# Kernel optimization log

Hardware: AMD Instinct MI355X
Metric: run time of the kernel (lower is better)

## Reference

```python
import jax, jax.numpy as jnp
import numpy as np


def setup_inputs() -> dict:
    key = jax.random.key(0)
    kq, kk, kv = jax.random.split(key, 3)
    N, L, S, H, D = 4, 2048, 2048, 8, 64
    queries = jax.random.normal(kq, (N, L, H, D), dtype=jnp.float32)
    keys = jax.random.normal(kk, (N, S, H, D), dtype=jnp.float32)
    values = jax.random.normal(kv, (N, S, H, D), dtype=jnp.float32)
    return {"queries": queries, "keys": keys, "values": values}


def reference(queries, keys, values):
    # QK^T: [N, L, S, H]
    qk = jnp.einsum('nlhd,nshd->nlsh', queries, keys)
    softmax_temp = 1.0 / np.sqrt(queries.shape[3]).astype(np.float32)
    attn = jax.nn.softmax(softmax_temp * qk, axis=2)  # softmax over S
    # dropout with drop_rate=0.0 is identity
    out = jnp.einsum('nlsh,nshd->nlhd', attn, values)
    return out
```

## Files before the change

kernel.cpp:

```cpp
#include <hip/hip_runtime.h>
#include <hip/hip_bf16.h>
#include <stdint.h>


typedef __bf16 bf16x8 __attribute__((ext_vector_type(8)));
typedef float  f32x16 __attribute__((ext_vector_type(16)));
typedef float  f32x2  __attribute__((ext_vector_type(2)));

#define QBLK 128
#define NT32 64
#define TILE32 4096
#define PLANE_BF16 (NT32 * TILE32)
#define SCALE_LOG2E 0.18033688011112042f

static __device__ __forceinline__ uint32_t pkbf(float lo, float hi) {
    uint16_t l = __builtin_bit_cast(uint16_t, (__bf16)lo);
    uint16_t h = __builtin_bit_cast(uint16_t, (__bf16)hi);
    return (uint32_t)l | ((uint32_t)h << 16);
}

static __device__ __forceinline__ bf16x8 packP8(float a0, float a1, float a2, float a3,
                                                float a4, float a5, float a6, float a7) {
    uint32_t x0 = pkbf(a0, a1), x1 = pkbf(a2, a3);
    uint32_t y0 = pkbf(a4, a5), y1 = pkbf(a6, a7);
    asm volatile("v_permlane32_swap_b32 %0, %1" : "+v"(x0), "+v"(y0));
    asm volatile("v_permlane32_swap_b32 %0, %1" : "+v"(x1), "+v"(y1));
    union { uint32_t u[4]; bf16x8 v; } pu;
    pu.u[0] = x0; pu.u[1] = x1; pu.u[2] = y0; pu.u[3] = y1;
    return pu.v;
}

__global__ __launch_bounds__(256) void prep(const float* __restrict__ K,
                                            const float* __restrict__ V,
                                            __bf16* __restrict__ F) {
    __shared__ __align__(16) __bf16 T[64 * 64];
    const int tid = threadIdx.x;
    if (blockIdx.x < 2048) {
        const int ch   = blockIdx.x * 256 + tid;
        const int nh   = ch >> 14;
        const int r    = ch & 16383;
        const int t    = r >> 8;
        const int rr   = r & 255;
        const int sl   = rr >> 3;
        const int slot = rr & 7;
        const int n = nh >> 3, h = nh & 7;
        const float* p = K + ((size_t)(n * 2048 + t * 32 + sl) * 8 + h) * 64 + slot * 8;
        float4 a = *(const float4*)p;
        float4 b = *(const float4*)(p + 4);
        bf16x8 v;
        v[0] = (__bf16)a.x; v[1] = (__bf16)a.y; v[2] = (__bf16)a.z; v[3] = (__bf16)a.w;
        v[4] = (__bf16)b.x; v[5] = (__bf16)b.y; v[6] = (__bf16)b.z; v[7] = (__bf16)b.w;
        const int ks = slot >> 1, hh = slot & 1;
        *(bf16x8*)(F + (size_t)nh * PLANE_BF16 + t * TILE32
                     + ks * 512 + (hh * 32 + sl) * 8) = v;
    } else {
        const int bid = blockIdx.x - 2048;
        const int nh  = bid >> 5;
        const int t0  = (bid & 31) * 2;
        const int n   = nh >> 3, h = nh & 7;
        const int s0  = (bid & 31) * 64;
#pragma unroll
        for (int it = 0; it < 16; ++it) {
            const int idx = it * 256 + tid;
            const int sl  = idx >> 6;
            const int d   = idx & 63;
            float v = V[(size_t)(n * 2048 + s0 + sl) * 512 + h * 64 + d];
            T[d * 64 + (((sl >> 3) ^ (d & 7)) * 8) + (sl & 7)] = (__bf16)v;
        }
        __syncthreads();
#pragma unroll
        for (int it = 0; it < 2; ++it) {
            const int idx = it * 256 + tid;
            const int d   = idx >> 3;
            const int sc  = idx & 7;
            bf16x8 v = *(const bf16x8*)&T[d * 64 + ((sc ^ (d & 7)) * 8)];
            const int dt = d >> 5, c = d & 31;
            const int tile = t0 + (sc >> 2), kt = (sc >> 1) & 1, hh = sc & 1;
            *(bf16x8*)(F + (size_t)nh * PLANE_BF16 + tile * TILE32
                         + (4 + dt * 2 + kt) * 512 + (hh * 32 + c) * 8) = v;
        }
    }
}

__global__ __launch_bounds__(512, 4) void fattn(const float* __restrict__ Q,
                                                const __bf16* __restrict__ F,
                                                float* __restrict__ Out) {
    __shared__ __align__(16) float Olds[4][32][64];
    __shared__ float Llds[8][32];

    const int tid  = threadIdx.x;
    const int wv   = tid >> 6;
    const int lane = tid & 63;
    const int hh   = lane >> 5;
    const int c    = lane & 31;
    const int part = wv >> 2;
    const int wq   = wv & 3;

    int bid = blockIdx.x;
    bid = (bid & 7) * 64 + (bid >> 3);
    const int nh = bid >> 4;
    const int qt = bid & 15;
    const int n  = nh >> 3, hd = nh & 7;
    const int q0 = qt * QBLK;
    const int t0 = part * 32;

    const float*  Qp = Q + (size_t)n * 1048576 + hd * 64;
    const bf16x8* Tb = (const bf16x8*)(F + (size_t)nh * PLANE_BF16);

    bf16x8 qf[4];
    {
        const float* qp = Qp + (size_t)(q0 + wq * 32 + c) * 512;
#pragma unroll
        for (int ks = 0; ks < 4; ++ks) {
            float4 a = *(const float4*)(qp + ks * 16 + hh * 8);
            float4 b = *(const float4*)(qp + ks * 16 + hh * 8 + 4);
            bf16x8 v;
            v[0] = (__bf16)(a.x * SCALE_LOG2E); v[1] = (__bf16)(a.y * SCALE_LOG2E);
            v[2] = (__bf16)(a.z * SCALE_LOG2E); v[3] = (__bf16)(a.w * SCALE_LOG2E);
            v[4] = (__bf16)(b.x * SCALE_LOG2E); v[5] = (__bf16)(b.y * SCALE_LOG2E);
            v[6] = (__bf16)(b.z * SCALE_LOG2E); v[7] = (__bf16)(b.w * SCALE_LOG2E);
            qf[ks] = v;
        }
    }

    f32x2 la0 = {0.f, 0.f}, la1 = {0.f, 0.f}, la2 = {0.f, 0.f}, la3 = {0.f, 0.f};
    f32x16 oacc[2];
#pragma unroll
    for (int dt = 0; dt < 2; ++dt)
#pragma unroll
        for (int r = 0; r < 16; ++r) oacc[dt][r] = 0.f;

    bf16x8 kA[4], vv[4];
#pragma unroll
    for (int f = 0; f < 4; ++f) {
        kA[f] = Tb[(size_t)t0 * 512 + f * 64 + lane];
        vv[f] = Tb[(size_t)t0 * 512 + 256 + f * 64 + lane];
    }

#pragma unroll 1
    for (int t = t0; t < t0 + 31; ++t) {
        f32x16 sacc;
#pragma unroll
        for (int r = 0; r < 16; ++r) sacc[r] = 0.f;
        __builtin_amdgcn_s_setprio(1);
#pragma unroll
        for (int ks = 0; ks < 4; ++ks)
            sacc = __builtin_amdgcn_mfma_f32_32x32x16_bf16(kA[ks], qf[ks], sacc, 0, 0, 0);
        __builtin_amdgcn_s_setprio(0);
#pragma unroll
        for (int f = 0; f < 4; ++f) kA[f] = Tb[(size_t)(t + 1) * 512 + f * 64 + lane];

#pragma unroll
        for (int r = 0; r < 8; ++r) sacc[r] = __builtin_amdgcn_exp2f(sacc[r]);
        bf16x8 pf0 = packP8(sacc[0], sacc[1], sacc[2], sacc[3],
                            sacc[4], sacc[5], sacc[6], sacc[7]);
        __builtin_amdgcn_s_setprio(1);
        oacc[0] = __builtin_amdgcn_mfma_f32_32x32x16_bf16(vv[0], pf0, oacc[0], 0, 0, 0);
        oacc[1] = __builtin_amdgcn_mfma_f32_32x32x16_bf16(vv[2], pf0, oacc[1], 0, 0, 0);
        __builtin_amdgcn_s_setprio(0);

#pragma unroll
        for (int r = 8; r < 16; ++r) sacc[r] = __builtin_amdgcn_exp2f(sacc[r]);
        bf16x8 pf1 = packP8(sacc[8],  sacc[9],  sacc[10], sacc[11],
                            sacc[12], sacc[13], sacc[14], sacc[15]);
        __builtin_amdgcn_s_setprio(1);
        oacc[0] = __builtin_amdgcn_mfma_f32_32x32x16_bf16(vv[1], pf1, oacc[0], 0, 0, 0);
        oacc[1] = __builtin_amdgcn_mfma_f32_32x32x16_bf16(vv[3], pf1, oacc[1], 0, 0, 0);
        __builtin_amdgcn_s_setprio(0);

        la0 += f32x2{sacc[0], sacc[1]} + f32x2{sacc[8],  sacc[9]};
        la1 += f32x2{sacc[2], sacc[3]} + f32x2{sacc[10], sacc[11]};
        la2 += f32x2{sacc[4], sacc[5]} + f32x2{sacc[12], sacc[13]};
        la3 += f32x2{sacc[6], sacc[7]} + f32x2{sacc[14], sacc[15]};

#pragma unroll
        for (int f = 0; f < 4; ++f) vv[f] = Tb[(size_t)(t + 1) * 512 + 256 + f * 64 + lane];
    }
    {
        f32x16 sacc;
#pragma unroll
        for (int r = 0; r < 16; ++r) sacc[r] = 0.f;
        __builtin_amdgcn_s_setprio(1);
#pragma unroll
        for (int ks = 0; ks < 4; ++ks)
            sacc = __builtin_amdgcn_mfma_f32_32x32x16_bf16(kA[ks], qf[ks], sacc, 0, 0, 0);
        __builtin_amdgcn_s_setprio(0);
#pragma unroll
        for (int r = 0; r < 8; ++r) sacc[r] = __builtin_amdgcn_exp2f(sacc[r]);
        bf16x8 pf0 = packP8(sacc[0], sacc[1], sacc[2], sacc[3],
                            sacc[4], sacc[5], sacc[6], sacc[7]);
        __builtin_amdgcn_s_setprio(1);
        oacc[0] = __builtin_amdgcn_mfma_f32_32x32x16_bf16(vv[0], pf0, oacc[0], 0, 0, 0);
        oacc[1] = __builtin_amdgcn_mfma_f32_32x32x16_bf16(vv[2], pf0, oacc[1], 0, 0, 0);
        __builtin_amdgcn_s_setprio(0);
#pragma unroll
        for (int r = 8; r < 16; ++r) sacc[r] = __builtin_amdgcn_exp2f(sacc[r]);
        bf16x8 pf1 = packP8(sacc[8],  sacc[9],  sacc[10], sacc[11],
                            sacc[12], sacc[13], sacc[14], sacc[15]);
        __builtin_amdgcn_s_setprio(1);
        oacc[0] = __builtin_amdgcn_mfma_f32_32x32x16_bf16(vv[1], pf1, oacc[0], 0, 0, 0);
        oacc[1] = __builtin_amdgcn_mfma_f32_32x32x16_bf16(vv[3], pf1, oacc[1], 0, 0, 0);
        __builtin_amdgcn_s_setprio(0);
        la0 += f32x2{sacc[0], sacc[1]} + f32x2{sacc[8],  sacc[9]};
        la1 += f32x2{sacc[2], sacc[3]} + f32x2{sacc[10], sacc[11]};
        la2 += f32x2{sacc[4], sacc[5]} + f32x2{sacc[12], sacc[13]};
        la3 += f32x2{sacc[6], sacc[7]} + f32x2{sacc[14], sacc[15]};
    }

    la0 += la1; la2 += la3; la0 += la2;
    float lsum = la0[0] + la0[1];
    lsum += __shfl_xor(lsum, 32, 64);
    if (hh == 0) Llds[wv][c] = lsum;
    if (part == 1) {
#pragma unroll
        for (int dt = 0; dt < 2; ++dt) {
#pragma unroll
            for (int rr = 0; rr < 4; ++rr) {
                const int s = dt * 8 + rr * 2 + hh;
                float4 o = { oacc[dt][4 * rr + 0], oacc[dt][4 * rr + 1],
                             oacc[dt][4 * rr + 2], oacc[dt][4 * rr + 3] };
                *(float4*)&Olds[wq][c][(s ^ (c & 15)) * 4] = o;
            }
        }
    }
    __syncthreads();
    if (part == 0) {
        const float lB  = Llds[wq + 4][c];
        const float inv = 1.0f / (lsum + lB);
        float* op = Out + (size_t)n * 1048576 + hd * 64 + (size_t)(q0 + wq * 32 + c) * 512;
#pragma unroll
        for (int dt = 0; dt < 2; ++dt) {
#pragma unroll
            for (int rr = 0; rr < 4; ++rr) {
                const int s = dt * 8 + rr * 2 + hh;
                float4 b = *(const float4*)&Olds[wq][c][(s ^ (c & 15)) * 4];
                float4 o = { (oacc[dt][4 * rr + 0] + b.x) * inv,
                             (oacc[dt][4 * rr + 1] + b.y) * inv,
                             (oacc[dt][4 * rr + 2] + b.z) * inv,
                             (oacc[dt][4 * rr + 3] + b.w) * inv };
                *(float4*)(op + dt * 32 + rr * 8 + hh * 4) = o;
            }
        }
    }
}

extern "C" void kernel_launch(void* const* d_in, const int* in_sizes, int n_in,
                              void* d_out, int out_size, void* d_ws, size_t ws_size,
                              hipStream_t stream) {
    const float* Q = (const float*)d_in[0];
    const float* K = (const float*)d_in[1];
    const float* V = (const float*)d_in[2];
    float* Out = (float*)d_out;
    __bf16* F = (__bf16*)d_ws;

    prep <<<dim3(3072), dim3(256), 0, stream>>>(K, V, F);
    fattn<<<dim3(512),  dim3(512), 0, stream>>>(Q, F, Out);
}
```

Measured before the change: 61.16 us.

## Double-buffer score tiles and halve query block per workgroup

New measurement: 63.97 us. +4.6%, slower.

```diff
diff --git a/kernel.cpp b/kernel.cpp
--- a/kernel.cpp
+++ b/kernel.cpp
@@ -7,7 +7,7 @@
 typedef float  f32x16 __attribute__((ext_vector_type(16)));
 typedef float  f32x2  __attribute__((ext_vector_type(2)));
 
-#define QBLK 128
+#define QBLK 64
 #define NT32 64
 #define TILE32 4096
 #define PLANE_BF16 (NT32 * TILE32)
@@ -82,24 +82,24 @@
     }
 }
 
-__global__ __launch_bounds__(512, 4) void fattn(const float* __restrict__ Q,
+__global__ __launch_bounds__(256, 3) void fattn(const float* __restrict__ Q,
                                                 const __bf16* __restrict__ F,
                                                 float* __restrict__ Out) {
-    __shared__ __align__(16) float Olds[4][32][64];
-    __shared__ float Llds[8][32];
+    __shared__ __align__(16) float Olds[2][32][64];
+    __shared__ float Llds[4][32];
 
     const int tid  = threadIdx.x;
     const int wv   = tid >> 6;
     const int lane = tid & 63;
     const int hh   = lane >> 5;
     const int c    = lane & 31;
-    const int part = wv >> 2;
-    const int wq   = wv & 3;
+    const int part = wv >> 1;
+    const int wq   = wv & 1;
 
     int bid = blockIdx.x;
-    bid = (bid & 7) * 64 + (bid >> 3);
-    const int nh = bid >> 4;
-    const int qt = bid & 15;
+    bid = (bid & 7) * 128 + (bid >> 3);
+    const int nh = bid >> 5;
+    const int qt = bid & 31;
     const int n  = nh >> 3, hd = nh & 7;
     const int q0 = qt * QBLK;
     const int t0 = part * 32;
@@ -131,81 +131,65 @@
         for (int r = 0; r < 16; ++r) oacc[dt][r] = 0.f;
 
     bf16x8 kA[4], vv[4];
-#pragma unroll
-    for (int f = 0; f < 4; ++f) {
-        kA[f] = Tb[(size_t)t0 * 512 + f * 64 + lane];
-        vv[f] = Tb[(size_t)t0 * 512 + 256 + f * 64 + lane];
-    }
-
-#pragma unroll 1
-    for (int t = t0; t < t0 + 31; ++t) {
-        f32x16 sacc;
-#pragma unroll
-        for (int r = 0; r < 16; ++r) sacc[r] = 0.f;
+
+    auto LK = [&](int tile) {
+#pragma unroll
+        for (int f = 0; f < 4; ++f) kA[f] = Tb[(size_t)tile * 512 + f * 64 + lane];
+    };
+    auto LV = [&](int tile) {
+#pragma unroll
+        for (int f = 0; f < 4; ++f) vv[f] = Tb[(size_t)tile * 512 + 256 + f * 64 + lane];
+    };
+    auto QK = [&](f32x16& s) {
+#pragma unroll
+        for (int r = 0; r < 16; ++r) s[r] = 0.f;
         __builtin_amdgcn_s_setprio(1);
 #pragma unroll
         for (int ks = 0; ks < 4; ++ks)
-            sacc = __builtin_amdgcn_mfma_f32_32x32x16_bf16(kA[ks], qf[ks], sacc, 0, 0, 0);
+            s = __builtin_amdgcn_mfma_f32_32x32x16_bf16(kA[ks], qf[ks], s, 0, 0, 0);
         __builtin_amdgcn_s_setprio(0);
-#pragma unroll
-        for (int f = 0; f < 4; ++f) kA[f] = Tb[(size_t)(t + 1) * 512 + f * 64 + lane];
-
-#pragma unroll
-        for (int r = 0; r < 8; ++r) sacc[r] = __builtin_amdgcn_exp2f(sacc[r]);
-        bf16x8 pf0 = packP8(sacc[0], sacc[1], sacc[2], sacc[3],
-                            sacc[4], sacc[5], sacc[6], sacc[7]);
+    };
+    auto SMPV = [&](f32x16& s) {
+#pragma unroll
+        for (int r = 0; r < 8; ++r) s[r] = __builtin_amdgcn_exp2f(s[r]);
+        bf16x8 pf0 = packP8(s[0], s[1], s[2], s[3], s[4], s[5], s[6], s[7]);
         __builtin_amdgcn_s_setprio(1);
         oacc[0] = __builtin_amdgcn_mfma_f32_32x32x16_bf16(vv[0], pf0, oacc[0], 0, 0, 0);
         oacc[1] = __builtin_amdgcn_mfma_f32_32x32x16_bf16(vv[2], pf0, oacc[1], 0, 0, 0);
         __builtin_amdgcn_s_setprio(0);
-
-#pragma unroll
-        for (int r = 8; r < 16; ++r) sacc[r] = __builtin_amdgcn_exp2f(sacc[r]);
-        bf16x8 pf1 = packP8(sacc[8],  sacc[9],  sacc[10], sacc[11],
-                            sacc[12], sacc[13], sacc[14], sacc[15]);
+#pragma unroll
+        for (int r = 8; r < 16; ++r) s[r] = __builtin_amdgcn_exp2f(s[r]);
+        bf16x8 pf1 = packP8(s[8], s[9], s[10], s[11], s[12], s[13], s[14], s[15]);
         __builtin_amdgcn_s_setprio(1);
         oacc[0] = __builtin_amdgcn_mfma_f32_32x32x16_bf16(vv[1], pf1, oacc[0], 0, 0, 0);
         oacc[1] = __builtin_amdgcn_mfma_f32_32x32x16_bf16(vv[3], pf1, oacc[1], 0, 0, 0);
         __builtin_amdgcn_s_setprio(0);
-
-        la0 += f32x2{sacc[0], sacc[1]} + f32x2{sacc[8],  sacc[9]};
-        la1 += f32x2{sacc[2], sacc[3]} + f32x2{sacc[10], sacc[11]};
-        la2 += f32x2{sacc[4], sacc[5]} + f32x2{sacc[12], sacc[13]};
-        la3 += f32x2{sacc[6], sacc[7]} + f32x2{sacc[14], sacc[15]};
-
-#pragma unroll
-        for (int f = 0; f < 4; ++f) vv[f] = Tb[(size_t)(t + 1) * 512 + 256 + f * 64 + lane];
-    }
-    {
-        f32x16 sacc;
-#pragma unroll
-        for (int r = 0; r < 16; ++r) sacc[r] = 0.f;
-        __builtin_amdgcn_s_setprio(1);
-#pragma unroll
-        for (int ks = 0; ks < 4; ++ks)
-            sacc = __builtin_amdgcn_mfma_f32_32x32x16_bf16(kA[ks], qf[ks], sacc, 0, 0, 0);
-        __builtin_amdgcn_s_setprio(0);
-#pragma unroll
-        for (int r = 0; r < 8; ++r) sacc[r] = __builtin_amdgcn_exp2f(sacc[r]);
-        bf16x8 pf0 = packP8(sacc[0], sacc[1], sacc[2], sacc[3],
-                            sacc[4], sacc[5], sacc[6], sacc[7]);
-        __builtin_amdgcn_s_setprio(1);
-        oacc[0] = __builtin_amdgcn_mfma_f32_32x32x16_bf16(vv[0], pf0, oacc[0], 0, 0, 0);
-        oacc[1] = __builtin_amdgcn_mfma_f32_32x32x16_bf16(vv[2], pf0, oacc[1], 0, 0, 0);
-        __builtin_amdgcn_s_setprio(0);
-#pragma unroll
-        for (int r = 8; r < 16; ++r) sacc[r] = __builtin_amdgcn_exp2f(sacc[r]);
-        bf16x8 pf1 = packP8(sacc[8],  sacc[9],  sacc[10], sacc[11],
-                            sacc[12], sacc[13], sacc[14], sacc[15]);
-        __builtin_amdgcn_s_setprio(1);
-        oacc[0] = __builtin_amdgcn_mfma_f32_32x32x16_bf16(vv[1], pf1, oacc[0], 0, 0, 0);
-        oacc[1] = __builtin_amdgcn_mfma_f32_32x32x16_bf16(vv[3], pf1, oacc[1], 0, 0, 0);
-        __builtin_amdgcn_s_setprio(0);
-        la0 += f32x2{sacc[0], sacc[1]} + f32x2{sacc[8],  sacc[9]};
-        la1 += f32x2{sacc[2], sacc[3]} + f32x2{sacc[10], sacc[11]};
-        la2 += f32x2{sacc[4], sacc[5]} + f32x2{sacc[12], sacc[13]};
-        la3 += f32x2{sacc[6], sacc[7]} + f32x2{sacc[14], sacc[15]};
-    }
+        la0 += f32x2{s[0], s[1]} + f32x2{s[8],  s[9]};
+        la1 += f32x2{s[2], s[3]} + f32x2{s[10], s[11]};
+        la2 += f32x2{s[4], s[5]} + f32x2{s[12], s[13]};
+        la3 += f32x2{s[6], s[7]} + f32x2{s[14], s[15]};
+    };
+
+    f32x16 sA, sB;
+    LK(t0); LV(t0);
+    QK(sA);
+    LK(t0 + 1);
+#pragma unroll 1
+    for (int i = 0; i < 15; ++i) {
+        const int t = t0 + 2 * i;
+        QK(sB);
+        LK(t + 2);
+        SMPV(sA);
+        LV(t + 1);
+        QK(sA);
+        LK(t + 3);
+        SMPV(sB);
+        LV(t + 2);
+    }
+    QK(sB);
+    SMPV(sA);
+    LV(t0 + 31);
+    SMPV(sB);
 
     la0 += la1; la2 += la3; la0 += la2;
     float lsum = la0[0] + la0[1];
@@ -225,7 +209,7 @@
     }
     __syncthreads();
     if (part == 0) {
-        const float lB  = Llds[wq + 4][c];
+        const float lB  = Llds[2 + wq][c];
         const float inv = 1.0f / (lsum + lB);
         float* op = Out + (size_t)n * 1048576 + hd * 64 + (size_t)(q0 + wq * 32 + c) * 512;
 #pragma unroll
@@ -254,5 +238,5 @@
     __bf16* F = (__bf16*)d_ws;
 
     prep <<<dim3(3072), dim3(256), 0, stream>>>(K, V, F);
-    fattn<<<dim3(512),  dim3(512), 0, stream>>>(Q, F, Out);
-}
+    fattn<<<dim3(1024), dim3(256), 0, stream>>>(Q, F, Out);
+}
```
